# Optimization experiments

Measured on AMD Instinct MI355X. Metric: run time of the kernel, lower is better.

Reference implementation:

```python
import jax, jax.numpy as jnp
from jax import lax
import numpy as np

EPS = 1e-5  # BatchNorm eps (eval mode, fresh running stats: mean=0, var=1)

N, T, H, C = 16, 512, 64, 64
O, K, E = 64, 9, 256


def setup_inputs() -> dict:
    key = jax.random.key(0)
    ks = jax.random.split(key, 16)
    X = jax.random.normal(ks[0], (N, T, H, C), dtype=jnp.float32)
    edges = jax.random.randint(ks[1], (N, 2, E), 0, H, dtype=jnp.int64)
    # att1/att2: Conv2d(C,1,1) == dot over channels + bias
    w_att1 = jax.random.normal(ks[2], (C,), jnp.float32) * (1.0 / np.sqrt(C))
    b_att1 = jax.random.normal(ks[3], (), jnp.float32) * 0.01
    w_att2 = jax.random.normal(ks[4], (C,), jnp.float32) * (1.0 / np.sqrt(C))
    b_att2 = jax.random.normal(ks[5], (), jnp.float32) * 0.01
    # GCN linear
    W_lin = jax.random.normal(ks[6], (O, C), jnp.float32) * (1.0 / np.sqrt(C))
    b_lin = jax.random.normal(ks[7], (O,), jnp.float32) * 0.01
    # tcn: BN -> ReLU -> Conv2d(O,O,(K,1)) -> BN -> Dropout(eval=id)
    bn1_gamma = 1.0 + 0.1 * jax.random.normal(ks[8], (O,), jnp.float32)
    bn1_beta = 0.1 * jax.random.normal(ks[9], (O,), jnp.float32)
    W_tcn = jax.random.normal(ks[10], (O, O, K, 1), jnp.float32) * (1.0 / np.sqrt(O * K))
    b_tcn = jax.random.normal(ks[11], (O,), jnp.float32) * 0.01
    bn2_gamma = 1.0 + 0.1 * jax.random.normal(ks[12], (O,), jnp.float32)
    bn2_beta = 0.1 * jax.random.normal(ks[13], (O,), jnp.float32)
    return dict(X=X, edges=edges, w_att1=w_att1, b_att1=b_att1, w_att2=w_att2,
                b_att2=b_att2, W_lin=W_lin, b_lin=b_lin, bn1_gamma=bn1_gamma,
                bn1_beta=bn1_beta, W_tcn=W_tcn, b_tcn=b_tcn,
                bn2_gamma=bn2_gamma, bn2_beta=bn2_beta)


def _bn_eval(x, gamma, beta):
    # eval-mode BatchNorm2d with running_mean=0, running_var=1; x is (N, Cc, T, H)
    inv = gamma / jnp.sqrt(1.0 + EPS)
    return x * inv[None, :, None, None] + beta[None, :, None, None]


def _forward(X, edges, w_att1, b_att1, w_att2, b_att2, W_lin, b_lin,
             bn1_gamma, bn1_beta, W_tcn, b_tcn, bn2_gamma, bn2_beta):
    n, t, h, c = X.shape
    k = W_tcn.shape[2]
    # --- adjacency from edge lists (duplicates sum, as sparse_coo->to_dense) ---
    bidx = jnp.arange(n)[:, None]
    adj = jnp.zeros((n, h, h), X.dtype).at[bidx, edges[:, 0, :], edges[:, 1, :]].add(1.0)
    # --- attention: a1[n,t,h] + a2[n,t,h'], leaky_relu, softmax over h ---
    a1 = jnp.einsum('nthc,c->nth', X, w_att1) + b_att1
    a2 = jnp.einsum('nthc,c->nth', X, w_att2) + b_att2
    s = jax.nn.leaky_relu(a1[:, :, :, None] + a2[:, :, None, :], 0.01)  # (n,t,h,h')
    att = jax.nn.softmax(s, axis=2)  # softmax over h (dim=1 pre-permute)
    # --- GCN: einsum('nthh,ntho->ntho') only uses diag(adj@att + I) ---
    diag = jnp.einsum('nhk,ntkh->nth', adj, att) + 1.0
    support = jnp.einsum('nthc,oc->ntho', X, W_lin) + b_lin  # (n,t,h,O)
    g = diag[..., None] * support
    # --- tcn: BN -> ReLU -> temporal conv (K,1) -> BN -> Dropout(eval) ---
    y = jnp.transpose(g, (0, 3, 1, 2))  # (n,O,t,h)
    y = jax.nn.relu(_bn_eval(y, bn1_gamma, bn1_beta))
    pad = (k - 1) // 2
    y = lax.conv_general_dilated(y, W_tcn, window_strides=(1, 1),
                                 padding=[(pad, pad), (0, 0)])
    y = y + b_tcn[None, :, None, None]
    y = _bn_eval(y, bn2_gamma, bn2_beta)
    # --- residual (identity: in==out, stride=1) + relu ---
    y = y + jnp.transpose(X, (0, 3, 1, 2))
    return jnp.transpose(jax.nn.relu(y), (0, 2, 3, 1))  # (n,t,h,O)


def reference(X, edges, w_att1, b_att1, w_att2, b_att2, W_lin, b_lin,
              bn1_gamma, bn1_beta, W_tcn, b_tcn, bn2_gamma, bn2_beta):
    return _forward(X, edges, w_att1, b_att1, w_att2, b_att2, W_lin, b_lin,
                    bn1_gamma, bn1_beta, W_tcn, b_tcn, bn2_gamma, bn2_beta)
```

## Files before the change

### kernel.cpp

```cpp
#include <hip/hip_runtime.h>
#include <hip/hip_bf16.h>
#include <stdint.h>

typedef float f32x4 __attribute__((ext_vector_type(4)));
typedef __bf16 bf16x8 __attribute__((ext_vector_type(8)));
typedef __bf16 bf16x4 __attribute__((ext_vector_type(4)));
typedef unsigned short u16;
typedef unsigned int u32;

__device__ __forceinline__ u16 f2bf(float f) {
    u32 u = __float_as_uint(f);
    u32 r = (u + 0x7fffu + ((u >> 16) & 1u)) >> 16;
    return (u16)r;
}

template <int CTRL>
__device__ __forceinline__ float rrot(float x) {
    int r = __builtin_amdgcn_update_dpp(0, __builtin_bit_cast(int, x), CTRL, 0xF, 0xF, false);
    return __builtin_bit_cast(float, r);
}
__device__ __forceinline__ float rowsum16(float p) {
    p += rrot<0x128>(p);
    p += rrot<0x124>(p);
    p += rrot<0x122>(p);
    p += rrot<0x121>(p);
    return p;
}

#define NB_ATTN 2048

__global__ __launch_bounds__(256) void k_attn(
    const float* __restrict__ X, const int* __restrict__ edges,
    const float* __restrict__ w1g, const float* __restrict__ b1g,
    const float* __restrict__ w2g, const float* __restrict__ b2g,
    const float* __restrict__ Wlin, const float* __restrict__ Wtcn,
    const float* __restrict__ blin, const float* __restrict__ g1,
    const float* __restrict__ be1, const float* __restrict__ btcn,
    const float* __restrict__ g2, const float* __restrict__ be2,
    u16* __restrict__ wlin_p, u16* __restrict__ wtcn_p,
    float* __restrict__ aux, float* __restrict__ diag) {
    const int tid = threadIdx.x;
    const int bid = blockIdx.x;
    const float rsf = 1.0f / sqrtf(1.0f + 1e-5f);

    if (bid >= NB_ATTN) {
        int idx = (bid - NB_ATTN) * 256 + tid;
        if (idx < 4096) {
            int jj = idx & 7, l = (idx >> 3) & 63, j = (idx >> 9) & 3, s = idx >> 11;
            int o = j * 16 + (l & 15);
            int c = s * 32 + (l >> 4) * 8 + jj;
            wlin_p[idx] = f2bf(Wlin[o * 64 + c] * (g1[o] * rsf));
        }
        int i2 = idx - 4096;
        if (i2 >= 0 && i2 < 36864) {
            int jj = i2 & 7, l = (i2 >> 3) & 63, j = (i2 >> 9) & 3, s = (i2 >> 11) & 1, kk = i2 >> 12;
            int o = j * 16 + (l & 15);
            int op = s * 32 + (l >> 4) * 8 + jj;
            wtcn_p[i2] = f2bf(Wtcn[(o * 64 + op) * 9 + kk] * (g2[o] * rsf));
        }
        if (idx >= 40960 && tid < 64) {
            aux[tid] = blin[tid] * g1[tid] * rsf;
            aux[64 + tid] = be1[tid];
            aux[128 + tid] = btcn[tid] * g2[tid] * rsf + be2[tid];
        }
        return;
    }

    __shared__ __align__(16) float adjT[64 * 65];
    __shared__ __align__(16) float A1s[4][64], A2s[4][64];

    const int n = bid >> 7;
    const int tg = bid & 127;
    const int w = tid >> 6, l = tid & 63;
    const int t = tg * 4 + w;
    const int c4 = l & 15, q = l >> 4;

    {
        f32x4 z4 = {0.f, 0.f, 0.f, 0.f};
        for (int i = tid; i < 1040; i += 256) *(f32x4*)(&adjT[i * 4]) = z4;
    }
    __syncthreads();
    {
        int r = edges[n * 512 + tid];
        int c = edges[n * 512 + 256 + tid];
        atomicAdd(&adjT[c * 65 + r], 1.0f);
    }

    const float* Xt = X + (size_t)(n * 512 + t) * 4096;
    const float4 w1v = *(const float4*)(w1g + c4 * 4);
    const float4 w2v = *(const float4*)(w2g + c4 * 4);
    float a1h = 0.f, a2h = 0.f;
#pragma unroll 8
    for (int i = 0; i < 16; i++) {
        float4 xv = *(const float4*)(Xt + (i * 64 + l) * 4);
        float p1 = xv.x * w1v.x + xv.y * w1v.y + xv.z * w1v.z + xv.w * w1v.w;
        float p2 = xv.x * w2v.x + xv.y * w2v.y + xv.z * w2v.z + xv.w * w2v.w;
        p1 = rowsum16(p1);
        p2 = rowsum16(p2);
        if (c4 == i) { a1h = p1; a2h = p2; }
    }
    {
        int hh = c4 * 4 + q;
        A1s[w][hh] = a1h + b1g[0];
        A2s[w][hh] = a2h + b2g[0];
    }
    __syncthreads();

    {
        float a2 = A2s[w][l];
        float num = 0.f, den = 0.f;
#pragma unroll
        for (int k4 = 0; k4 < 16; k4++) {
            float4 a1v = *(const float4*)(&A1s[w][k4 * 4]);
#pragma unroll
            for (int j = 0; j < 4; j++) {
                int k = k4 * 4 + j;
                float s = ((const float*)&a1v)[j] + a2;
                s = fmaxf(s, 0.01f * s);
                float e = __expf(s);
                den += e;
                num = fmaf(adjT[k * 65 + l], e, num);
            }
        }
        diag[((size_t)(n * 64 + l)) * 512 + t] = num / den + 1.0f;
    }
}

__global__ __launch_bounds__(256) void k_gcn_tcn(
    const float* __restrict__ X, const float* __restrict__ diag,
    const u16* __restrict__ wlin_p, const u16* __restrict__ wtcn_p,
    const float* __restrict__ aux, float* __restrict__ out) {
    __shared__ __align__(16) u16 As[144 * 72];
    __shared__ float DGs[144];

    const int tid = threadIdx.x;
    const int bid = blockIdx.x;
    const int n = bid >> 8, h = (bid >> 2) & 63, tb = (bid & 3) * 128;
    const float* Xbase = X + ((size_t)(n * 512) * 64 + h) * 64;

#pragma unroll
    for (int i = 0; i < 9; i++) {
        int idx = tid + 256 * i;
        int r = idx >> 4, c4 = idx & 15;
        int tg = tb - 4 + r;
        float4 xv = make_float4(0.f, 0.f, 0.f, 0.f);
        if (tg >= 0 && tg < 512) xv = *(const float4*)(Xbase + (size_t)tg * 4096 + c4 * 4);
        bf16x4 pk;
        pk[0] = (__bf16)xv.x; pk[1] = (__bf16)xv.y;
        pk[2] = (__bf16)xv.z; pk[3] = (__bf16)xv.w;
        *(bf16x4*)(&As[r * 72 + c4 * 4]) = pk;
    }
    if (tid < 144) {
        int tg = tb - 4 + tid;
        DGs[tid] = (tg >= 0 && tg < 512) ? diag[((size_t)(n * 64 + h)) * 512 + tg] : 0.f;
    }

    const int w = tid >> 6, l = tid & 63;
    const int col = l & 15, q = l >> 4;
    const f32x4 zv = {0.f, 0.f, 0.f, 0.f};

    float blp[4], bb1[4], cc2[4];
#pragma unroll
    for (int j = 0; j < 4; j++) {
        int o = 16 * j + col;
        blp[j] = aux[o];
        bb1[j] = aux[64 + o];
        cc2[j] = aux[128 + o];
    }
    __syncthreads();

    for (int mt = w; mt < 9; mt += 4) {
        f32x4 acc[4] = {zv, zv, zv, zv};
#pragma unroll
        for (int s = 0; s < 2; s++) {
            bf16x8 a = *(const bf16x8*)(&As[(16 * mt + col) * 72 + s * 32 + q * 8]);
#pragma unroll
            for (int j = 0; j < 4; j++) {
                bf16x8 b = *(const bf16x8*)(&wlin_p[((s * 4 + j) * 64 + l) * 8]);
                acc[j] = __builtin_amdgcn_mfma_f32_16x16x32_bf16(a, b, acc[j], 0, 0, 0);
            }
        }
#pragma unroll
        for (int j = 0; j < 4; j++) {
#pragma unroll
            for (int rr = 0; rr < 4; rr++) {
                int row = 16 * mt + q * 4 + rr;
                int tg = tb - 4 + row;
                float v = fmaf(acc[j][rr] + blp[j], DGs[row], bb1[j]);
                v = v > 0.f ? v : 0.f;
                if (tg < 0 || tg >= 512) v = 0.f;
                __bf16 bv = (__bf16)v;
                As[row * 72 + 16 * j + col] = __builtin_bit_cast(u16, bv);
            }
        }
    }
    __syncthreads();

    f32x4 acc2[2][4];
#pragma unroll
    for (int mt = 0; mt < 2; mt++)
#pragma unroll
        for (int j = 0; j < 4; j++) acc2[mt][j] = zv;

    for (int kk = 0; kk < 9; kk++) {
#pragma unroll
        for (int s = 0; s < 2; s++) {
            bf16x8 b[4];
#pragma unroll
            for (int j = 0; j < 4; j++)
                b[j] = *(const bf16x8*)(&wtcn_p[(((kk * 2 + s) * 4 + j) * 64 + l) * 8]);
            bf16x8 a[2];
#pragma unroll
            for (int mt = 0; mt < 2; mt++) {
                int row = 32 * w + 16 * mt + col + kk;
                a[mt] = *(const bf16x8*)(&As[row * 72 + s * 32 + q * 8]);
            }
#pragma unroll
            for (int mt = 0; mt < 2; mt++)
#pragma unroll
                for (int j = 0; j < 4; j++)
                    acc2[mt][j] = __builtin_amdgcn_mfma_f32_16x16x32_bf16(a[mt], b[j], acc2[mt][j], 0, 0, 0);
        }
    }

#pragma unroll
    for (int mt = 0; mt < 2; mt++) {
        float res[4][4];
#pragma unroll
        for (int rr = 0; rr < 4; rr++) {
            int tt = tb + 32 * w + 16 * mt + 4 * q + rr;
#pragma unroll
            for (int j = 0; j < 4; j++)
                res[j][rr] = X[((size_t)(n * 512 + tt) * 64 + h) * 64 + 16 * j + col];
        }
#pragma unroll
        for (int rr = 0; rr < 4; rr++) {
            int tt = tb + 32 * w + 16 * mt + 4 * q + rr;
#pragma unroll
            for (int j = 0; j < 4; j++) {
                size_t off = ((size_t)(n * 512 + tt) * 64 + h) * 64 + 16 * j + col;
                float v = acc2[mt][j][rr] + cc2[j] + res[j][rr];
                out[off] = v > 0.f ? v : 0.f;
            }
        }
    }
}

extern "C" void kernel_launch(void* const* d_in, const int* in_sizes, int n_in,
                              void* d_out, int out_size, void* d_ws, size_t ws_size,
                              hipStream_t stream) {
    const float* X    = (const float*)d_in[0];
    const int*  edges = (const int*)d_in[1];
    const float* w1   = (const float*)d_in[2];
    const float* b1   = (const float*)d_in[3];
    const float* w2   = (const float*)d_in[4];
    const float* b2   = (const float*)d_in[5];
    const float* Wlin = (const float*)d_in[6];
    const float* blin = (const float*)d_in[7];
    const float* g1   = (const float*)d_in[8];
    const float* be1  = (const float*)d_in[9];
    const float* Wtcn = (const float*)d_in[10];
    const float* btcn = (const float*)d_in[11];
    const float* g2   = (const float*)d_in[12];
    const float* be2  = (const float*)d_in[13];
    float* out = (float*)d_out;

    char* ws = (char*)d_ws;
    u16*   wlin_p = (u16*)ws;
    u16*   wtcn_p = (u16*)(ws + 8192);
    float* aux    = (float*)(ws + 8192 + 73728);
    float* diag   = (float*)(ws + 8192 + 73728 + 1024);

    hipLaunchKernelGGL(k_attn, dim3(NB_ATTN + 161), dim3(256), 0, stream,
                       X, edges, w1, b1, w2, b2, Wlin, Wtcn,
                       blin, g1, be1, btcn, g2, be2,
                       wlin_p, wtcn_p, aux, diag);
    hipLaunchKernelGGL(k_gcn_tcn, dim3(16 * 64 * 4), dim3(256), 0, stream,
                       X, diag, wlin_p, wtcn_p, aux, out);
}
```

Baseline: 319.8 us.

## Stage bf16 copy of X in attention pass and prefetch residual early

The attention kernel now writes a bf16 copy of X to workspace while it streams X, and the GCN/TCN kernel loads its halo tile from that half-width copy instead of re-reading fp32 X and converting. Residual X values are also loaded before the TCN MFMA loop so their latency overlaps compute. The change adds a 64 MB write to the first kernel and more live registers in the second, in exchange for halving the bytes read for the tile (the tile is re-read about 1.06x due to the halo). It only runs if the workspace is large enough.

```diff
diff --git a/kernel.cpp b/kernel.cpp
--- a/kernel.cpp
+++ b/kernel.cpp
@@ -29,6 +29,7 @@
 
 #define NB_ATTN 2048
 
+template <bool WB>
 __global__ __launch_bounds__(256) void k_attn(
     const float* __restrict__ X, const int* __restrict__ edges,
     const float* __restrict__ w1g, const float* __restrict__ b1g,
@@ -38,7 +39,8 @@
     const float* __restrict__ be1, const float* __restrict__ btcn,
     const float* __restrict__ g2, const float* __restrict__ be2,
     u16* __restrict__ wlin_p, u16* __restrict__ wtcn_p,
-    float* __restrict__ aux, float* __restrict__ diag) {
+    float* __restrict__ aux, float* __restrict__ diag,
+    u16* __restrict__ Xbf) {
     const int tid = threadIdx.x;
     const int bid = blockIdx.x;
     const float rsf = 1.0f / sqrtf(1.0f + 1e-5f);
@@ -87,12 +89,19 @@
     }
 
     const float* Xt = X + (size_t)(n * 512 + t) * 4096;
+    u16* Xbt = WB ? (Xbf + (size_t)(n * 512 + t) * 4096) : nullptr;
     const float4 w1v = *(const float4*)(w1g + c4 * 4);
     const float4 w2v = *(const float4*)(w2g + c4 * 4);
     float a1h = 0.f, a2h = 0.f;
 #pragma unroll 8
     for (int i = 0; i < 16; i++) {
         float4 xv = *(const float4*)(Xt + (i * 64 + l) * 4);
+        if (WB) {
+            bf16x4 pk;
+            pk[0] = (__bf16)xv.x; pk[1] = (__bf16)xv.y;
+            pk[2] = (__bf16)xv.z; pk[3] = (__bf16)xv.w;
+            *(bf16x4*)(Xbt + (i * 64 + l) * 4) = pk;
+        }
         float p1 = xv.x * w1v.x + xv.y * w1v.y + xv.z * w1v.z + xv.w * w1v.w;
         float p2 = xv.x * w2v.x + xv.y * w2v.y + xv.z * w2v.z + xv.w * w2v.w;
         p1 = rowsum16(p1);
@@ -126,8 +135,10 @@
     }
 }
 
+template <bool BF>
 __global__ __launch_bounds__(256) void k_gcn_tcn(
-    const float* __restrict__ X, const float* __restrict__ diag,
+    const float* __restrict__ X, const u16* __restrict__ Xbf,
+    const float* __restrict__ diag,
     const u16* __restrict__ wlin_p, const u16* __restrict__ wtcn_p,
     const float* __restrict__ aux, float* __restrict__ out) {
     __shared__ __align__(16) u16 As[144 * 72];
@@ -136,19 +147,32 @@
     const int tid = threadIdx.x;
     const int bid = blockIdx.x;
     const int n = bid >> 8, h = (bid >> 2) & 63, tb = (bid & 3) * 128;
-    const float* Xbase = X + ((size_t)(n * 512) * 64 + h) * 64;
-
-#pragma unroll
-    for (int i = 0; i < 9; i++) {
-        int idx = tid + 256 * i;
-        int r = idx >> 4, c4 = idx & 15;
-        int tg = tb - 4 + r;
-        float4 xv = make_float4(0.f, 0.f, 0.f, 0.f);
-        if (tg >= 0 && tg < 512) xv = *(const float4*)(Xbase + (size_t)tg * 4096 + c4 * 4);
-        bf16x4 pk;
-        pk[0] = (__bf16)xv.x; pk[1] = (__bf16)xv.y;
-        pk[2] = (__bf16)xv.z; pk[3] = (__bf16)xv.w;
-        *(bf16x4*)(&As[r * 72 + c4 * 4]) = pk;
+
+    if (BF) {
+        const u16* Xb = Xbf + (size_t)(n * 512) * 4096 + h * 64;
+#pragma unroll
+        for (int i = 0; i < 9; i++) {
+            int idx = tid + 256 * i;
+            int r = idx >> 4, c4 = idx & 15;
+            int tg = tb - 4 + r;
+            uint2 d = make_uint2(0u, 0u);
+            if (tg >= 0 && tg < 512) d = *(const uint2*)(Xb + (size_t)tg * 4096 + c4 * 4);
+            *(uint2*)(&As[r * 72 + c4 * 4]) = d;
+        }
+    } else {
+        const float* Xbase = X + ((size_t)(n * 512) * 64 + h) * 64;
+#pragma unroll
+        for (int i = 0; i < 9; i++) {
+            int idx = tid + 256 * i;
+            int r = idx >> 4, c4 = idx & 15;
+            int tg = tb - 4 + r;
+            float4 xv = make_float4(0.f, 0.f, 0.f, 0.f);
+            if (tg >= 0 && tg < 512) xv = *(const float4*)(Xbase + (size_t)tg * 4096 + c4 * 4);
+            bf16x4 pk;
+            pk[0] = (__bf16)xv.x; pk[1] = (__bf16)xv.y;
+            pk[2] = (__bf16)xv.z; pk[3] = (__bf16)xv.w;
+            *(bf16x4*)(&As[r * 72 + c4 * 4]) = pk;
+        }
     }
     if (tid < 144) {
         int tg = tb - 4 + tid;
@@ -196,6 +220,17 @@
     }
     __syncthreads();
 
+    float res[2][4][4];
+#pragma unroll
+    for (int mt = 0; mt < 2; mt++)
+#pragma unroll
+        for (int rr = 0; rr < 4; rr++) {
+            int tt = tb + 32 * w + 16 * mt + 4 * q + rr;
+#pragma unroll
+            for (int j = 0; j < 4; j++)
+                res[mt][j][rr] = X[((size_t)(n * 512 + tt) * 64 + h) * 64 + 16 * j + col];
+        }
+
     f32x4 acc2[2][4];
 #pragma unroll
     for (int mt = 0; mt < 2; mt++)
@@ -225,21 +260,13 @@
 
 #pragma unroll
     for (int mt = 0; mt < 2; mt++) {
-        float res[4][4];
 #pragma unroll
         for (int rr = 0; rr < 4; rr++) {
             int tt = tb + 32 * w + 16 * mt + 4 * q + rr;
 #pragma unroll
-            for (int j = 0; j < 4; j++)
-                res[j][rr] = X[((size_t)(n * 512 + tt) * 64 + h) * 64 + 16 * j + col];
-        }
-#pragma unroll
-        for (int rr = 0; rr < 4; rr++) {
-            int tt = tb + 32 * w + 16 * mt + 4 * q + rr;
-#pragma unroll
             for (int j = 0; j < 4; j++) {
                 size_t off = ((size_t)(n * 512 + tt) * 64 + h) * 64 + 16 * j + col;
-                float v = acc2[mt][j][rr] + cc2[j] + res[j][rr];
+                float v = acc2[mt][j][rr] + cc2[j] + res[mt][j][rr];
                 out[off] = v > 0.f ? v : 0.f;
             }
         }
@@ -270,11 +297,22 @@
     u16*   wtcn_p = (u16*)(ws + 8192);
     float* aux    = (float*)(ws + 8192 + 73728);
     float* diag   = (float*)(ws + 8192 + 73728 + 1024);
-
-    hipLaunchKernelGGL(k_attn, dim3(NB_ATTN + 161), dim3(256), 0, stream,
-                       X, edges, w1, b1, w2, b2, Wlin, Wtcn,
-                       blin, g1, be1, btcn, g2, be2,
-                       wlin_p, wtcn_p, aux, diag);
-    hipLaunchKernelGGL(k_gcn_tcn, dim3(16 * 64 * 4), dim3(256), 0, stream,
-                       X, diag, wlin_p, wtcn_p, aux, out);
-}
+    u16*   Xbf    = (u16*)(ws + 8192 + 73728 + 1024 + 2097152);
+    const size_t need = 8192 + 73728 + 1024 + 2097152 + 67108864;
+
+    if (ws_size >= need) {
+        hipLaunchKernelGGL((k_attn<true>), dim3(NB_ATTN + 161), dim3(256), 0, stream,
+                           X, edges, w1, b1, w2, b2, Wlin, Wtcn,
+                           blin, g1, be1, btcn, g2, be2,
+                           wlin_p, wtcn_p, aux, diag, Xbf);
+        hipLaunchKernelGGL((k_gcn_tcn<true>), dim3(16 * 64 * 4), dim3(256), 0, stream,
+                           X, Xbf, diag, wlin_p, wtcn_p, aux, out);
+    } else {
+        hipLaunchKernelGGL((k_attn<false>), dim3(NB_ATTN + 161), dim3(256), 0, stream,
+                           X, edges, w1, b1, w2, b2, Wlin, Wtcn,
+                           blin, g1, be1, btcn, g2, be2,
+                           wlin_p, wtcn_p, aux, diag, (u16*)nullptr);
+        hipLaunchKernelGGL((k_gcn_tcn<false>), dim3(16 * 64 * 4), dim3(256), 0, stream,
+                           X, (const u16*)nullptr, diag, wlin_p, wtcn_p, aux, out);
+    }
+}
```

After: 344.7 us. 1.08x slower.

## Halve time tile in gcn_tcn kernel and split output channels across waves

Applied to the files above, without the earlier changes.

The fused GCN+TCN kernel now handles 64 time steps per block instead of 128, doubling the grid, shrinking shared memory, and adding a launch-bounds occupancy hint. In the temporal conv each wave now owns one 16-channel output slice across all four time subtiles, instead of a 32-row time slice across all channels. This should cut LDS and registers per block and raise occupancy. The cost is a larger halo overhead (8 extra rows per 64 instead of per 128), so more redundant X loads and first-stage GEMM work.

```diff
diff --git a/kernel.cpp b/kernel.cpp
--- a/kernel.cpp
+++ b/kernel.cpp
@@ -126,20 +126,20 @@
     }
 }
 
-__global__ __launch_bounds__(256) void k_gcn_tcn(
+__global__ __launch_bounds__(256, 6) void k_gcn_tcn(
     const float* __restrict__ X, const float* __restrict__ diag,
     const u16* __restrict__ wlin_p, const u16* __restrict__ wtcn_p,
     const float* __restrict__ aux, float* __restrict__ out) {
-    __shared__ __align__(16) u16 As[144 * 72];
-    __shared__ float DGs[144];
+    __shared__ __align__(16) u16 As[80 * 72];
+    __shared__ float DGs[80];
 
     const int tid = threadIdx.x;
     const int bid = blockIdx.x;
-    const int n = bid >> 8, h = (bid >> 2) & 63, tb = (bid & 3) * 128;
+    const int n = bid >> 9, h = (bid >> 3) & 63, tb = (bid & 7) * 64;
     const float* Xbase = X + ((size_t)(n * 512) * 64 + h) * 64;
 
 #pragma unroll
-    for (int i = 0; i < 9; i++) {
+    for (int i = 0; i < 5; i++) {
         int idx = tid + 256 * i;
         int r = idx >> 4, c4 = idx & 15;
         int tg = tb - 4 + r;
@@ -150,7 +150,7 @@
         pk[2] = (__bf16)xv.z; pk[3] = (__bf16)xv.w;
         *(bf16x4*)(&As[r * 72 + c4 * 4]) = pk;
     }
-    if (tid < 144) {
+    if (tid < 80) {
         int tg = tb - 4 + tid;
         DGs[tid] = (tg >= 0 && tg < 512) ? diag[((size_t)(n * 64 + h)) * 512 + tg] : 0.f;
     }
@@ -159,17 +159,17 @@
     const int col = l & 15, q = l >> 4;
     const f32x4 zv = {0.f, 0.f, 0.f, 0.f};
 
-    float blp[4], bb1[4], cc2[4];
+    float blp[4], bb1[4];
 #pragma unroll
     for (int j = 0; j < 4; j++) {
         int o = 16 * j + col;
         blp[j] = aux[o];
         bb1[j] = aux[64 + o];
-        cc2[j] = aux[128 + o];
-    }
-    __syncthreads();
-
-    for (int mt = w; mt < 9; mt += 4) {
+    }
+    const float cc2 = aux[128 + 16 * w + col];
+    __syncthreads();
+
+    for (int mt = w; mt < 5; mt += 4) {
         f32x4 acc[4] = {zv, zv, zv, zv};
 #pragma unroll
         for (int s = 0; s < 2; s++) {
@@ -196,52 +196,34 @@
     }
     __syncthreads();
 
-    f32x4 acc2[2][4];
-#pragma unroll
-    for (int mt = 0; mt < 2; mt++)
-#pragma unroll
-        for (int j = 0; j < 4; j++) acc2[mt][j] = zv;
-
+    f32x4 acc2[4] = {zv, zv, zv, zv};
+#pragma unroll
     for (int kk = 0; kk < 9; kk++) {
 #pragma unroll
         for (int s = 0; s < 2; s++) {
-            bf16x8 b[4];
-#pragma unroll
-            for (int j = 0; j < 4; j++)
-                b[j] = *(const bf16x8*)(&wtcn_p[(((kk * 2 + s) * 4 + j) * 64 + l) * 8]);
-            bf16x8 a[2];
-#pragma unroll
-            for (int mt = 0; mt < 2; mt++) {
-                int row = 32 * w + 16 * mt + col + kk;
-                a[mt] = *(const bf16x8*)(&As[row * 72 + s * 32 + q * 8]);
-            }
-#pragma unroll
-            for (int mt = 0; mt < 2; mt++)
-#pragma unroll
-                for (int j = 0; j < 4; j++)
-                    acc2[mt][j] = __builtin_amdgcn_mfma_f32_16x16x32_bf16(a[mt], b[j], acc2[mt][j], 0, 0, 0);
-        }
-    }
-
-#pragma unroll
-    for (int mt = 0; mt < 2; mt++) {
-        float res[4][4];
+            bf16x8 b = *(const bf16x8*)(&wtcn_p[(((kk * 2 + s) * 4 + w) * 64 + l) * 8]);
+#pragma unroll
+            for (int mt = 0; mt < 4; mt++) {
+                bf16x8 a = *(const bf16x8*)(&As[(16 * mt + col + kk) * 72 + s * 32 + q * 8]);
+                acc2[mt] = __builtin_amdgcn_mfma_f32_16x16x32_bf16(a, b, acc2[mt], 0, 0, 0);
+            }
+        }
+    }
+
+#pragma unroll
+    for (int mt = 0; mt < 4; mt++) {
+        float res[4];
 #pragma unroll
         for (int rr = 0; rr < 4; rr++) {
-            int tt = tb + 32 * w + 16 * mt + 4 * q + rr;
-#pragma unroll
-            for (int j = 0; j < 4; j++)
-                res[j][rr] = X[((size_t)(n * 512 + tt) * 64 + h) * 64 + 16 * j + col];
+            int tt = tb + 16 * mt + 4 * q + rr;
+            res[rr] = X[((size_t)(n * 512 + tt) * 64 + h) * 64 + 16 * w + col];
         }
 #pragma unroll
         for (int rr = 0; rr < 4; rr++) {
-            int tt = tb + 32 * w + 16 * mt + 4 * q + rr;
-#pragma unroll
-            for (int j = 0; j < 4; j++) {
-                size_t off = ((size_t)(n * 512 + tt) * 64 + h) * 64 + 16 * j + col;
-                float v = acc2[mt][j][rr] + cc2[j] + res[j][rr];
-                out[off] = v > 0.f ? v : 0.f;
-            }
+            int tt = tb + 16 * mt + 4 * q + rr;
+            size_t off = ((size_t)(n * 512 + tt) * 64 + h) * 64 + 16 * w + col;
+            float v = acc2[mt][rr] + cc2 + res[rr];
+            out[off] = v > 0.f ? v : 0.f;
         }
     }
 }
@@ -275,6 +257,6 @@
                        X, edges, w1, b1, w2, b2, Wlin, Wtcn,
                        blin, g1, be1, btcn, g2, be2,
                        wlin_p, wtcn_p, aux, diag);
-    hipLaunchKernelGGL(k_gcn_tcn, dim3(16 * 64 * 4), dim3(256), 0, stream,
+    hipLaunchKernelGGL(k_gcn_tcn, dim3(16 * 64 * 8), dim3(256), 0, stream,
                        X, diag, wlin_p, wtcn_p, aux, out);
 }
```

Measured after the change: 343.4 us. +7.4%, slower.
